# Kernel tuning notes

Hardware: AMD Instinct MI355X
Metric: run time of the kernel (lower is better)

The kernel has to match this reference:

```python
import jax, jax.numpy as jnp
import numpy as np

B, T, E, H = 1024, 200, 128, 128
N_ITEMS, N_CATS = 100000, 1000
LN_EPS = 1e-5


def _prelu(x, a):
    return jnp.where(x >= 0, x, a * x)


def _layernorm(x, g, b):
    m = x.mean(-1, keepdims=True)
    v = ((x - m) ** 2).mean(-1, keepdims=True)
    return (x - m) / jnp.sqrt(v + LN_EPS) * g + b


def setup_inputs() -> dict:
    key = jax.random.key(0)
    it = iter(jax.random.split(key, 64))
    nx = lambda: next(it)
    def lin(out_d, in_d):
        s = 1.0 / np.sqrt(in_d)
        return jax.random.uniform(nx(), (out_d, in_d), jnp.float32, -s, s)
    inp = {}
    inp['behavior_ids'] = jax.random.randint(nx(), (B, T), 0, N_ITEMS)
    inp['candidate_id'] = jax.random.randint(nx(), (B,), 0, N_ITEMS)
    inp['candidate_cat'] = jax.random.randint(nx(), (B,), 0, N_CATS)
    inp['dense_features'] = jax.random.normal(nx(), (B, 5), jnp.float32)
    inp['item_emb'] = (jax.random.normal(nx(), (N_ITEMS, E), jnp.float32) * 0.01).at[0].set(0.0)
    inp['cat_emb'] = (jax.random.normal(nx(), (N_CATS, E // 2), jnp.float32) * 0.01).at[0].set(0.0)
    # nn.GRU params (gate order r,z,n)
    inp['gru_wih'] = lin(3 * H, E)
    inp['gru_whh'] = lin(3 * H, H)
    inp['gru_bih'] = jnp.zeros((3 * H,), jnp.float32)
    inp['gru_bhh'] = jnp.zeros((3 * H,), jnp.float32)
    # auxiliary_net: Linear(H,E) -> ReLU -> Linear(E,1)
    inp['aux_w1'] = lin(E, H); inp['aux_b1'] = jnp.zeros((E,), jnp.float32)
    inp['aux_w2'] = lin(1, E); inp['aux_b2'] = jnp.zeros((1,), jnp.float32)
    # attention_mlp: Linear(3H,64) -> PReLU -> Linear(64,1)
    inp['att_w1'] = lin(64, 3 * H); inp['att_b1'] = jnp.zeros((64,), jnp.float32)
    inp['att_a'] = jnp.array(0.25, jnp.float32)
    inp['att_w2'] = lin(1, 64); inp['att_b2'] = jnp.zeros((1,), jnp.float32)
    # AUGRU gates: Linear(2H, H) each
    inp['wz'] = lin(H, 2 * H); inp['bz'] = jnp.zeros((H,), jnp.float32)
    inp['wr'] = lin(H, 2 * H); inp['br'] = jnp.zeros((H,), jnp.float32)
    inp['wh'] = lin(H, 2 * H); inp['bh'] = jnp.zeros((H,), jnp.float32)
    # dense_proj Linear(5,32)
    inp['dp_w'] = lin(32, 5); inp['dp_b'] = jnp.zeros((32,), jnp.float32)
    # MLP: 352 -> 256 -> 128 -> 64, each Linear + LayerNorm + PReLU
    dims = [H + E + E // 2 + 32, 256, 128, 64]
    for i in range(3):
        inp[f'm_w{i+1}'] = lin(dims[i + 1], dims[i])
        inp[f'm_b{i+1}'] = jnp.zeros((dims[i + 1],), jnp.float32)
        inp[f'ln_g{i+1}'] = jnp.ones((dims[i + 1],), jnp.float32)
        inp[f'ln_b{i+1}'] = jnp.zeros((dims[i + 1],), jnp.float32)
        inp[f'pa{i+1}'] = jnp.array(0.25, jnp.float32)
    # 3 task heads Linear(64,1), stacked
    inp['heads_w'] = lin(3, 64); inp['heads_b'] = jnp.zeros((3,), jnp.float32)
    return inp


def _forward_core(behavior_ids, candidate_id, candidate_cat, dense_features,
                  item_emb, cat_emb, gru_wih, gru_whh, gru_bih, gru_bhh,
                  aux_w1, aux_b1, aux_w2, aux_b2,
                  att_w1, att_b1, att_a, att_w2, att_b2,
                  wz, bz, wr, br, wh, bh, dp_w, dp_b,
                  m_w1, m_b1, ln_g1, ln_b1, pa1,
                  m_w2, m_b2, ln_g2, ln_b2, pa2,
                  m_w3, m_b3, ln_g3, ln_b3, pa3,
                  heads_w, heads_b):
    beh = item_emb[behavior_ids]            # [B,T,E]
    cand = item_emb[candidate_id]           # [B,E]
    catv = cat_emb[candidate_cat]           # [B,E//2]
    Bsz = beh.shape[0]
    Hd = gru_whh.shape[1]
    h0 = jnp.zeros((Bsz, Hd), beh.dtype)
    # --- interest extractor GRU (cuDNN GRU math, gate order r,z,n) ---
    xp = jnp.einsum('bte,ge->btg', beh, gru_wih) + gru_bih  # [B,T,3H]
    def gru_step(h, x):
        hp = h @ gru_whh.T + gru_bhh
        xr, xz, xn = jnp.split(x, 3, -1)
        hr, hz, hn = jnp.split(hp, 3, -1)
        r = jax.nn.sigmoid(xr + hr)
        z = jax.nn.sigmoid(xz + hz)
        n = jnp.tanh(xn + r * hn)
        hnew = (1 - z) * n + z * h
        return hnew, hnew
    _, hs = jax.lax.scan(gru_step, h0, jnp.swapaxes(xp, 0, 1))
    hs = jnp.swapaxes(hs, 0, 1)             # [B,T,H]
    # --- auxiliary logits ---
    aux = jax.nn.relu(hs[:, :-1] @ aux_w1.T + aux_b1) @ aux_w2.T + aux_b2  # [B,T-1,1]
    # --- attention (embed_dim == hidden_size so cand_proj == candidate_emb) ---
    ce = cand[:, None, :]
    att_in = jnp.concatenate([hs, jnp.broadcast_to(ce, hs.shape), hs * ce], -1)  # [B,T,3H]
    scores = (_prelu(att_in @ att_w1.T + att_b1, att_a) @ att_w2.T + att_b2)[..., 0]
    att = jax.nn.softmax(scores, axis=-1)   # [B,T]
    # --- AUGRU: attention-modulated update gate ---
    def augru_step(h, xs):
        x, a = xs                           # x: [B,H], a: [B]
        comb = jnp.concatenate([x, h], -1)
        z = jax.nn.sigmoid(comb @ wz.T + bz)
        r = jax.nn.sigmoid(comb @ wr.T + br)
        comb_r = jnp.concatenate([x, r * h], -1)
        ht = jnp.tanh(comb_r @ wh.T + bh)
        zp = a[:, None] * z
        return (1 - zp) * h + zp * ht, None
    hT, _ = jax.lax.scan(augru_step, h0, (jnp.swapaxes(hs, 0, 1), att.T))
    # --- fusion MLP (dropout is identity in eval) ---
    dense_out = dense_features @ dp_w.T + dp_b
    x = jnp.concatenate([hT, cand, catv, dense_out], -1)  # [B,352]
    for (w, b, g, be, a) in ((m_w1, m_b1, ln_g1, ln_b1, pa1),
                             (m_w2, m_b2, ln_g2, ln_b2, pa2),
                             (m_w3, m_b3, ln_g3, ln_b3, pa3)):
        x = _prelu(_layernorm(x @ w.T + b, g, be), a)
    preds = jax.nn.sigmoid(x @ heads_w.T + heads_b)  # [B,3] == 3 heads of [B,1]
    return preds, aux


def reference(behavior_ids, candidate_id, candidate_cat, dense_features,
              item_emb, cat_emb, gru_wih, gru_whh, gru_bih, gru_bhh,
              aux_w1, aux_b1, aux_w2, aux_b2,
              att_w1, att_b1, att_a, att_w2, att_b2,
              wz, bz, wr, br, wh, bh, dp_w, dp_b,
              m_w1, m_b1, ln_g1, ln_b1, pa1,
              m_w2, m_b2, ln_g2, ln_b2, pa2,
              m_w3, m_b3, ln_g3, ln_b3, pa3,
              heads_w, heads_b):
    return _forward_core(behavior_ids, candidate_id, candidate_cat, dense_features,
                         item_emb, cat_emb, gru_wih, gru_whh, gru_bih, gru_bhh,
                         aux_w1, aux_b1, aux_w2, aux_b2,
                         att_w1, att_b1, att_a, att_w2, att_b2,
                         wz, bz, wr, br, wh, bh, dp_w, dp_b,
                         m_w1, m_b1, ln_g1, ln_b1, pa1,
                         m_w2, m_b2, ln_g2, ln_b2, pa2,
                         m_w3, m_b3, ln_g3, ln_b3, pa3,
                         heads_w, heads_b)
```

## Files before the change

### kernel.cpp

```cpp
#include <hip/hip_runtime.h>


typedef __bf16 bf16;
typedef float f32x4 __attribute__((ext_vector_type(4)));
typedef __bf16 bf16x8 __attribute__((ext_vector_type(8)));
typedef __bf16 bf16x4 __attribute__((ext_vector_type(4)));

#define MFMA16(a, b, c) __builtin_amdgcn_mfma_f32_16x16x32_bf16((a), (b), (c), 0, 0, 0)

#define BATCH 1024
#define SEQT 200
#define F32_ONE 0x3F800000u

__device__ __forceinline__ float sigm(float x) {
  return __builtin_amdgcn_rcpf(1.0f + __expf(-x));
}
__device__ __forceinline__ float tanh_fast(float x) {
  float ax = fabsf(x);
  float t = 1.0f - 2.0f * __builtin_amdgcn_rcpf(__expf(2.0f * ax) + 1.0f);
  return copysignf(t, x);
}

__device__ __forceinline__ void bar_lgkm() {
  asm volatile("s_waitcnt lgkmcnt(0)\n\ts_barrier" ::: "memory");
}

__device__ __forceinline__ void dma16(const void* g, void* l) {
  __builtin_amdgcn_global_load_lds((__attribute__((address_space(1))) void*)g,
                                   (__attribute__((address_space(3))) void*)l,
                                   16, 0, 0);
}

template <typename DT> __device__ __forceinline__ float ldf(const DT* p, long i);
template <> __device__ __forceinline__ float ldf<bf16>(const bf16* p, long i) { return (float)p[i]; }
template <> __device__ __forceinline__ float ldf<float>(const float* p, long i) { return p[i]; }

template <typename DT> __device__ __forceinline__ bf16x8 ld8(const DT* p, long i);
template <> __device__ __forceinline__ bf16x8 ld8<bf16>(const bf16* p, long i) {
  return *(const bf16x8*)(p + i);
}
template <> __device__ __forceinline__ bf16x8 ld8<float>(const float* p, long i) {
  f32x4 a = *(const f32x4*)(p + i);
  f32x4 b = *(const f32x4*)(p + i + 4);
  bf16x8 r;
  r[0] = (bf16)a[0]; r[1] = (bf16)a[1]; r[2] = (bf16)a[2]; r[3] = (bf16)a[3];
  r[4] = (bf16)b[0]; r[5] = (bf16)b[1]; r[6] = (bf16)b[2]; r[7] = (bf16)b[3];
  return r;
}

template <typename DT>
__device__ __forceinline__ void prep_body(
    const int* __restrict__ cid, const int* __restrict__ ccat,
    const DT* __restrict__ dense, const DT* __restrict__ item_emb,
    const DT* __restrict__ cat_emb, const DT* __restrict__ dp_w,
    const DT* __restrict__ dp_b, bf16* __restrict__ candbuf, bf16* __restrict__ xf) {
  const int b = blockIdx.x;
  const int t = threadIdx.x;
  bf16 v = (bf16)ldf(item_emb, (long)cid[b] * 128 + t);
  candbuf[b * 128 + t] = v;
  xf[(long)b * 352 + 128 + t] = v;
  if (t < 64) xf[(long)b * 352 + 256 + t] = (bf16)ldf(cat_emb, (long)ccat[b] * 64 + t);
  if (t < 32) {
    float s = ldf(dp_b, t);
    for (int k = 0; k < 5; k++) s += ldf(dense, b * 5 + k) * ldf(dp_w, t * 5 + k);
    xf[(long)b * 352 + 320 + t] = (bf16)s;
  }
}
__global__ __launch_bounds__(128) void k_prep(
    const unsigned* __restrict__ disc, const int* cid, const int* ccat,
    const void* dense, const void* item_emb, const void* cat_emb,
    const void* dp_w, const void* dp_b, bf16* candbuf, bf16* xf) {
  if (*disc == F32_ONE)
    prep_body<float>(cid, ccat, (const float*)dense, (const float*)item_emb,
                     (const float*)cat_emb, (const float*)dp_w, (const float*)dp_b, candbuf, xf);
  else
    prep_body<bf16>(cid, ccat, (const bf16*)dense, (const bf16*)item_emb,
                    (const bf16*)cat_emb, (const bf16*)dp_w, (const bf16*)dp_b, candbuf, xf);
}

template <typename DT>
__device__ __forceinline__ void gru3_body(
    const int* __restrict__ ids, const DT* __restrict__ item_emb,
    const DT* __restrict__ wih, const DT* __restrict__ whh,
    const DT* __restrict__ bih, const DT* __restrict__ bhh, bf16* __restrict__ hs,
    bf16 (*hA)[16][136], bf16 (*xb)[4][16][136], char* raw) {
  const int b0 = blockIdx.x * 16;
  const int tid = threadIdx.x;
  const int w = tid >> 6, lane = tid & 63, l15 = lane & 15, quad = lane >> 4;
  const int nc = w * 16 + l15;

  for (int i = tid; i < 2 * 16 * 136; i += 512) ((bf16*)hA)[i] = (bf16)0.0f;

  bf16x8 wir[4], wiz[4], win_[4], whr[4], whz[4], whn[4];
#pragma unroll
  for (int k = 0; k < 4; k++) {
    const long off = k * 32 + quad * 8;
    wir[k] = ld8(wih, (long)nc * 128 + off);
    wiz[k] = ld8(wih, (long)(128 + nc) * 128 + off);
    win_[k] = ld8(wih, (long)(256 + nc) * 128 + off);
    whr[k] = ld8(whh, (long)nc * 128 + off);
    whz[k] = ld8(whh, (long)(128 + nc) * 128 + off);
    whn[k] = ld8(whh, (long)(256 + nc) * 128 + off);
  }
  const float br_s = ldf(bih, nc) + ldf(bhh, nc);
  const float bz_s = ldf(bih, 128 + nc) + ldf(bhh, 128 + nc);
  const float bxn_s = ldf(bih, 256 + nc);
  const float bhn_s = ldf(bhh, 256 + nc);

  const int idrow = (sizeof(DT) == 4) ? (tid >> 5) : ((tid >> 4) & 15);
  const int* idbase = ids + (long)(b0 + idrow) * SEQT;

  auto DMA = [&](const int4 id4) {
    if constexpr (sizeof(DT) == 4) {
#pragma unroll
      for (int j = 0; j < 4; j++)
        dma16((const char*)(item_emb + (long)((&id4.x)[j]) * 128) + (tid & 31) * 16,
              raw + (j * 512 + tid) * 16);
    } else {
#pragma unroll
      for (int j = 0; j < 2; j++) {
        const int slot = j * 2 + (tid >> 8);
        dma16((const char*)(item_emb + (long)((&id4.x)[slot]) * 128) + (tid & 15) * 16,
              raw + (j * 512 + tid) * 16);
      }
    }
  };
  auto CONV = [&](int buf) {
    if constexpr (sizeof(DT) == 4) {
      const float* rf = (const float*)raw;
#pragma unroll
      for (int h = 0; h < 4; h++) {
        const int e = h * 2048 + tid * 4;
        f32x4 a = *(const f32x4*)(rf + e);
        const int slot = e >> 11, row = (e >> 7) & 15, col = e & 127;
        bf16x4 o;
        o[0] = (bf16)a[0]; o[1] = (bf16)a[1]; o[2] = (bf16)a[2]; o[3] = (bf16)a[3];
        *(bf16x4*)&xb[buf][slot][row][col] = o;
      }
    } else {
      const bf16* rh = (const bf16*)raw;
#pragma unroll
      for (int h = 0; h < 2; h++) {
        const int e = h * 4096 + tid * 8;
        const int slot = e >> 11, row = (e >> 7) & 15, col = e & 127;
        *(bf16x8*)&xb[buf][slot][row][col] = *(const bf16x8*)(rh + e);
      }
    }
  };

  const int srow = tid >> 5, sch = (tid & 31) * 4;
  bf16* hsb = hs + ((long)(b0 + srow) * SEQT) * 128 + sch;

  float hreg[4] = {0.f, 0.f, 0.f, 0.f};
  const f32x4 z4 = {0.f, 0.f, 0.f, 0.f};

  int4 idv = *(const int4*)(idbase);
  DMA(idv);
  idv = *(const int4*)(idbase + 4);
  asm volatile("s_waitcnt vmcnt(1)" ::: "memory");
  __builtin_amdgcn_sched_barrier(0);
  __builtin_amdgcn_s_barrier();
  CONV(0);
  asm volatile("s_waitcnt lgkmcnt(0)" ::: "memory");
  __builtin_amdgcn_sched_barrier(0);
  __builtin_amdgcn_s_barrier();
  DMA(idv);
  idv = *(const int4*)(idbase + 8);

#define GRU_STEP(P, S)                                                         \
  {                                                                            \
    const int tt = t0 + (S);                                                   \
    bf16x8 af[4], xaf[4];                                                      \
    _Pragma("unroll") for (int k = 0; k < 4; k++) {                            \
      af[k] = *(const bf16x8*)&hA[P][l15][k * 32 + quad * 8];                  \
      xaf[k] = *(const bf16x8*)&xb[buf][S][l15][k * 32 + quad * 8];            \
    }                                                                          \
    { const int slot = tt ? tt - 1 : 0;                                        \
      bf16x4 hv = *(const bf16x4*)&hA[P][srow][sch];                           \
      *(bf16x4*)(hsb + (long)slot * 128) = hv; }                               \
    f32x4 ar = z4, az = z4, axn = z4, ahn = z4;                                \
    _Pragma("unroll") for (int k = 0; k < 4; k++) {                            \
      ar = MFMA16(xaf[k], wir[k], ar);                                         \
      az = MFMA16(xaf[k], wiz[k], az);                                         \
      axn = MFMA16(xaf[k], win_[k], axn);                                      \
    }                                                                          \
    _Pragma("unroll") for (int k = 0; k < 4; k++) {                            \
      ar = MFMA16(af[k], whr[k], ar);                                          \
      az = MFMA16(af[k], whz[k], az);                                          \
      ahn = MFMA16(af[k], whn[k], ahn);                                        \
    }                                                                          \
    _Pragma("unroll") for (int r = 0; r < 4; r++) {                            \
      float r_ = sigm(ar[r] + br_s);                                           \
      float z_ = sigm(az[r] + bz_s);                                           \
      float n_ = tanh_fast(axn[r] + bxn_s + r_ * (ahn[r] + bhn_s));            \
      float hnew = (1.0f - z_) * n_ + z_ * hreg[r];                            \
      hreg[r] = hnew;                                                          \
      hA[(P) ^ 1][quad * 4 + r][nc] = (bf16)hnew;                              \
    }                                                                          \
    bar_lgkm();                                                                \
  }

  for (int c = 0; c < 50; c++) {
    const int t0 = c * 4;
    const int buf = c & 1;
    GRU_STEP(0, 0) GRU_STEP(1, 1) GRU_STEP(0, 2) GRU_STEP(1, 3)
    if (c < 49) {
      asm volatile("s_waitcnt vmcnt(4)" ::: "memory");
      __builtin_amdgcn_sched_barrier(0);
      __builtin_amdgcn_s_barrier();
      CONV((c + 1) & 1);
      asm volatile("s_waitcnt lgkmcnt(0)" ::: "memory");
      __builtin_amdgcn_sched_barrier(0);
      __builtin_amdgcn_s_barrier();
      if (c < 48) {
        DMA(idv);
        int nid = (c + 3) * 4; if (nid > 196) nid = 196;
        idv = *(const int4*)(idbase + nid);
      }
    }
  }
#undef GRU_STEP
  { bf16x4 hv = *(const bf16x4*)&hA[0][srow][sch];
    *(bf16x4*)(hsb + (long)(SEQT - 1) * 128) = hv; }
}
__global__ __launch_bounds__(512, 1) void k_gru3(
    const unsigned* __restrict__ disc, const int* ids, const void* item_emb,
    const void* wih, const void* whh, const void* bih, const void* bhh, bf16* hs) {
  __shared__ __align__(16) bf16 hA[2][16][136];
  __shared__ __align__(16) bf16 xb[2][4][16][136];
  __shared__ __align__(16) char raw[32768];
  if (*disc == F32_ONE)
    gru3_body<float>(ids, (const float*)item_emb, (const float*)wih, (const float*)whh,
                     (const float*)bih, (const float*)bhh, hs, hA, xb, raw);
  else
    gru3_body<bf16>(ids, (const bf16*)item_emb, (const bf16*)wih, (const bf16*)whh,
                    (const bf16*)bih, (const bf16*)bhh, hs, hA, xb, raw);
}

template <typename DT>
__device__ __forceinline__ void attaux_body(
    const bf16* __restrict__ hs, const int* __restrict__ cid,
    const DT* __restrict__ item_emb,
    const DT* __restrict__ aw1, const DT* __restrict__ ab1,
    const DT* __restrict__ aw2, const DT* __restrict__ ab2,
    const DT* __restrict__ tw1, const DT* __restrict__ tb1, const DT* __restrict__ ta,
    const DT* __restrict__ tw2, const DT* __restrict__ tb2,
    float* __restrict__ sc, float* __restrict__ outaux,
    bf16 (*As)[64][128], float (*scPt)[64], float (*scPa)[64]) {
  const int t0 = blockIdx.x * 64;
  const int b0 = blockIdx.y * 16;
  const int tid = threadIdx.x, w = tid >> 6, lane = tid & 63, l15 = lane & 15, quad = lane >> 4;

  const int tn = w * 16 + l15;
  bf16x8 wth[4], wtc[4], wthc[4], wa0[4], wa1[4];
#pragma unroll
  for (int k = 0; k < 4; k++) {
    const long off = k * 32 + quad * 8;
    wth[k]  = ld8(tw1, (long)tn * 384 + off);
    wtc[k]  = ld8(tw1, (long)tn * 384 + 128 + off);
    wthc[k] = ld8(tw1, (long)tn * 384 + 256 + off);
    wa0[k]  = ld8(aw1, (long)((2 * w) * 16 + l15) * 128 + off);
    wa1[k]  = ld8(aw1, (long)((2 * w + 1) * 16 + l15) * 128 + off);
  }
  const float tb1c = ldf(tb1, tn), tw2c = ldf(tw2, tn);
  const float ab1c0 = ldf(ab1, (2 * w) * 16 + l15), aw2c0 = ldf(aw2, (2 * w) * 16 + l15);
  const float ab1c1 = ldf(ab1, (2 * w + 1) * 16 + l15), aw2c1 = ldf(aw2, (2 * w + 1) * 16 + l15);
  const float aP = ldf(ta, 0), tb2s = ldf(tb2, 0), ab2s = ldf(ab2, 0);

  auto DMA = [&](int b, int buf) {
#pragma unroll
    for (int c = 0; c < 4; c++) {
      const int idx = c * 256 + tid;
      const int row = idx >> 4, p = idx & 15;
      int t = t0 + row; if (t > SEQT - 1) t = SEQT - 1;
      const bf16* src = hs + ((long)b * SEQT + t) * 128 + ((p ^ (row & 7)) * 8);
      dma16(src, (char*)(&As[buf][0][0]) + idx * 16);
    }
  };
  auto CANDLD = [&](int b, bf16x8* cf) {
#pragma unroll
    for (int k = 0; k < 4; k++)
      cf[k] = ld8(item_emb, (long)cid[b] * 128 + k * 32 + quad * 8);
  };

  const f32x4 z4 = {0.f, 0.f, 0.f, 0.f};
  bf16x8 candA[4], candB[4];
  DMA(b0, 0);
  CANDLD(b0, candA);
  asm volatile("s_waitcnt vmcnt(0)" ::: "memory");
  __builtin_amdgcn_sched_barrier(0);
  __builtin_amdgcn_s_barrier();

#define AA_STEP(BI, CUSE, CPF)                                                 \
  {                                                                            \
    const int b = b0 + (BI);                                                   \
    const int buf = (BI) & 1;                                                  \
    if ((BI) + 1 < 16) { DMA(b + 1, buf ^ 1); CANDLD(b + 1, CPF); }            \
    _Pragma("unroll") for (int m = 0; m < 4; m++) {                            \
      const bf16* arow = &As[buf][m * 16 + l15][0];                            \
      bf16x8 af[4], hcf[4];                                                    \
      _Pragma("unroll") for (int k = 0; k < 4; k++)                            \
        af[k] = *(const bf16x8*)((const char*)arow +                           \
                                 (((k * 4 + quad) ^ (l15 & 7)) << 4));         \
      _Pragma("unroll") for (int k = 0; k < 4; k++)                            \
      _Pragma("unroll") for (int j = 0; j < 8; j++)                            \
        hcf[k][j] = (bf16)((float)af[k][j] * (float)CUSE[k][j]);               \
      f32x4 at = z4, aa0 = z4, aa1 = z4;                                       \
      _Pragma("unroll") for (int k = 0; k < 4; k++) {                          \
        at = MFMA16(af[k], wth[k], at);                                        \
        at = MFMA16(CUSE[k], wtc[k], at);                                      \
        at = MFMA16(hcf[k], wthc[k], at);                                      \
        aa0 = MFMA16(af[k], wa0[k], aa0);                                      \
        aa1 = MFMA16(af[k], wa1[k], aa1);                                      \
      }                                                                        \
      float tp[4], ap[4];                                                      \
      _Pragma("unroll") for (int r = 0; r < 4; r++) {                          \
        float y = at[r] + tb1c;                                                \
        y = (y >= 0.f) ? y : aP * y;                                           \
        tp[r] = y * tw2c;                                                      \
        float y0 = aa0[r] + ab1c0;                                             \
        float y1 = aa1[r] + ab1c1;                                             \
        ap[r] = (y0 > 0.f ? y0 : 0.f) * aw2c0 + (y1 > 0.f ? y1 : 0.f) * aw2c1; \
      }                                                                        \
      _Pragma("unroll") for (int mm = 1; mm < 16; mm <<= 1)                    \
      _Pragma("unroll") for (int r = 0; r < 4; r++) {                          \
        tp[r] += __shfl_xor(tp[r], mm, 64);                                    \
        ap[r] += __shfl_xor(ap[r], mm, 64);                                    \
      }                                                                        \
      if (l15 == 0) {                                                          \
        *(float4*)&scPt[w][m * 16 + quad * 4] =                                \
            make_float4(tp[0], tp[1], tp[2], tp[3]);                           \
        *(float4*)&scPa[w][m * 16 + quad * 4] =                                \
            make_float4(ap[0], ap[1], ap[2], ap[3]);                           \
      }                                                                        \
    }                                                                          \
    bar_lgkm();                                                                \
    if (tid < 64) {                                                            \
      int t = t0 + tid;                                                        \
      if (t < SEQT) {                                                          \
        float s = scPt[0][tid] + scPt[1][tid] + scPt[2][tid] + scPt[3][tid];   \
        sc[(long)b * SEQT + t] = s + tb2s;                                     \
      }                                                                        \
    } else if (tid < 128) {                                                    \
      int tt2 = tid - 64, t = t0 + tt2;                                        \
      if (t < SEQT - 1) {                                                      \
        float s = scPa[0][tt2] + scPa[1][tt2] + scPa[2][tt2] + scPa[3][tt2];   \
        outaux[(long)b * 199 + t] = s + ab2s;                                  \
      }                                                                        \
    }                                                                          \
    asm volatile("s_waitcnt vmcnt(0) lgkmcnt(0)" ::: "memory");                \
    __builtin_amdgcn_sched_barrier(0);                                         \
    __builtin_amdgcn_s_barrier();                                              \
  }

  for (int bi = 0; bi < 16; bi += 2) {
    AA_STEP(bi, candA, candB)
    AA_STEP(bi + 1, candB, candA)
  }
#undef AA_STEP
}
__global__ __launch_bounds__(256, 1) void k_attaux(
    const unsigned* __restrict__ disc, const bf16* hs, const int* cid,
    const void* item_emb,
    const void* aw1, const void* ab1, const void* aw2, const void* ab2,
    const void* tw1, const void* tb1, const void* ta, const void* tw2, const void* tb2,
    float* sc, float* outaux) {
  __shared__ __align__(16) bf16 As[2][64][128];
  __shared__ __align__(16) float scPt[4][64];
  __shared__ __align__(16) float scPa[4][64];
  if (*disc == F32_ONE)
    attaux_body<float>(hs, cid, (const float*)item_emb,
                       (const float*)aw1, (const float*)ab1, (const float*)aw2, (const float*)ab2,
                       (const float*)tw1, (const float*)tb1, (const float*)ta,
                       (const float*)tw2, (const float*)tb2, sc, outaux, As, scPt, scPa);
  else
    attaux_body<bf16>(hs, cid, (const bf16*)item_emb,
                      (const bf16*)aw1, (const bf16*)ab1, (const bf16*)aw2, (const bf16*)ab2,
                      (const bf16*)tw1, (const bf16*)tb1, (const bf16*)ta,
                      (const bf16*)tw2, (const bf16*)tb2, sc, outaux, As, scPt, scPa);
}

__global__ __launch_bounds__(256) void k_softmax(float* __restrict__ sc) {
  const int b = blockIdx.x, tid = threadIdx.x;
  __shared__ float red[256];
  float v = (tid < SEQT) ? sc[(long)b * SEQT + tid] : -1e30f;
  red[tid] = v; __syncthreads();
  for (int s = 128; s > 0; s >>= 1) { if (tid < s) red[tid] = fmaxf(red[tid], red[tid + s]); __syncthreads(); }
  float mx = red[0]; __syncthreads();
  float e = (tid < SEQT) ? __expf(v - mx) : 0.f;
  red[tid] = e; __syncthreads();
  for (int s = 128; s > 0; s >>= 1) { if (tid < s) red[tid] += red[tid + s]; __syncthreads(); }
  float inv = 1.0f / red[0];
  if (tid < SEQT) sc[(long)b * SEQT + tid] = e * inv;
}

template <typename DT>
__device__ __forceinline__ void augru3_body(
    const bf16* __restrict__ hsrc, const float* __restrict__ att,
    const DT* __restrict__ wz, const DT* __restrict__ wr, const DT* __restrict__ wh,
    const DT* __restrict__ bzv, const DT* __restrict__ brv, const DT* __restrict__ bhv,
    bf16* __restrict__ xf_out,
    bf16 (*hA)[16][136], bf16 (*rhA)[136], float (*attL)[201],
    bf16 (*xb)[4][16][136], char* raw) {
  const int b0 = blockIdx.x * 16;
  const int tid = threadIdx.x;
  const int w = tid >> 6, lane = tid & 63, l15 = lane & 15, quad = lane >> 4;
  const int nc = w * 16 + l15;

  for (int i = tid; i < 2 * 16 * 136; i += 512) ((bf16*)hA)[i] = (bf16)0.0f;
  for (int i = tid; i < 16 * SEQT; i += 512) {
    int r = i / SEQT, c = i - r * SEQT;
    attL[r][c] = att[(long)(b0 + r) * SEQT + c];
  }

  bf16x8 wzx[4], wzh[4], wrx[4], wrh[4], whx[4], whh_[4];
#pragma unroll
  for (int k = 0; k < 4; k++) {
    const long off = k * 32 + quad * 8;
    wzx[k] = ld8(wz, (long)nc * 256 + off);
    wzh[k] = ld8(wz, (long)nc * 256 + 128 + off);
    wrx[k] = ld8(wr, (long)nc * 256 + off);
    wrh[k] = ld8(wr, (long)nc * 256 + 128 + off);
    whx[k] = ld8(wh, (long)nc * 256 + off);
    whh_[k] = ld8(wh, (long)nc * 256 + 128 + off);
  }
  const float bz_s = ldf(bzv, nc);
  const float br_s = ldf(brv, nc);
  const float bh_s = ldf(bhv, nc);

  auto DMA = [&](int t0) {
#pragma unroll
    for (int j = 0; j < 2; j++) {
      const int slot = j * 2 + (tid >> 8);
      const int row = (tid >> 4) & 15;
      const bf16* src = hsrc + ((long)(b0 + row) * SEQT + t0 + slot) * 128 + (tid & 15) * 8;
      dma16(src, raw + (j * 512 + tid) * 16);
    }
  };
  auto CONV = [&](int buf) {
    const bf16* rh = (const bf16*)raw;
#pragma unroll
    for (int h = 0; h < 2; h++) {
      const int e = h * 4096 + tid * 8;
      const int slot = e >> 11, row = (e >> 7) & 15, col = e & 127;
      *(bf16x8*)&xb[buf][slot][row][col] = *(const bf16x8*)(rh + e);
    }
  };

  float hreg[4] = {0.f, 0.f, 0.f, 0.f};
  const f32x4 z4 = {0.f, 0.f, 0.f, 0.f};

  DMA(0);
  asm volatile("s_waitcnt vmcnt(0)" ::: "memory");
  __builtin_amdgcn_sched_barrier(0);
  __builtin_amdgcn_s_barrier();
  CONV(0);
  asm volatile("s_waitcnt lgkmcnt(0)" ::: "memory");
  __builtin_amdgcn_sched_barrier(0);
  __builtin_amdgcn_s_barrier();
  DMA(4);

#define AUGRU_STEP(P, S)                                                       \
  {                                                                            \
    const int tt = t0 + (S);                                                   \
    bf16x8 af[4], xaf[4];                                                      \
    _Pragma("unroll") for (int k = 0; k < 4; k++) {                            \
      af[k] = *(const bf16x8*)&hA[P][l15][k * 32 + quad * 8];                  \
      xaf[k] = *(const bf16x8*)&xb[buf][S][l15][k * 32 + quad * 8];            \
    }                                                                          \
    f32x4 az = z4, ar = z4, axh = z4;                                          \
    _Pragma("unroll") for (int k = 0; k < 4; k++) {                            \
      az = MFMA16(xaf[k], wzx[k], az);                                         \
      ar = MFMA16(xaf[k], wrx[k], ar);                                         \
      axh = MFMA16(xaf[k], whx[k], axh);                                       \
    }                                                                          \
    _Pragma("unroll") for (int k = 0; k < 4; k++) {                            \
      az = MFMA16(af[k], wzh[k], az);                                          \
      ar = MFMA16(af[k], wrh[k], ar);                                          \
    }                                                                          \
    float zp[4];                                                               \
    _Pragma("unroll") for (int r = 0; r < 4; r++) {                            \
      float a_ = attL[quad * 4 + r][tt];                                       \
      float z_ = sigm(az[r] + bz_s);                                           \
      float r_ = sigm(ar[r] + br_s);                                           \
      zp[r] = a_ * z_;                                                         \
      rhA[quad * 4 + r][nc] = (bf16)(r_ * hreg[r]);                            \
    }                                                                          \
    bar_lgkm();                                                                \
    bf16x8 rf[4];                                                              \
    _Pragma("unroll") for (int k = 0; k < 4; k++)                              \
      rf[k] = *(const bf16x8*)&rhA[l15][k * 32 + quad * 8];                    \
    f32x4 ahh = axh;                                                           \
    _Pragma("unroll") for (int k = 0; k < 4; k++)                              \
      ahh = MFMA16(rf[k], whh_[k], ahh);                                       \
    _Pragma("unroll") for (int r = 0; r < 4; r++) {                            \
      float ht = tanh_fast(ahh[r] + bh_s);                                     \
      float hnew = (1.f - zp[r]) * hreg[r] + zp[r] * ht;                       \
      hreg[r] = hnew;                                                          \
      hA[(P) ^ 1][quad * 4 + r][nc] = (bf16)hnew;                              \
    }                                                                          \
    bar_lgkm();                                                                \
  }

  for (int c = 0; c < 50; c++) {
    const int t0 = c * 4;
    const int buf = c & 1;
    AUGRU_STEP(0, 0) AUGRU_STEP(1, 1) AUGRU_STEP(0, 2) AUGRU_STEP(1, 3)
    if (c < 49) {
      asm volatile("s_waitcnt vmcnt(0)" ::: "memory");
      __builtin_amdgcn_sched_barrier(0);
      __builtin_amdgcn_s_barrier();
      CONV((c + 1) & 1);
      asm volatile("s_waitcnt lgkmcnt(0)" ::: "memory");
      __builtin_amdgcn_sched_barrier(0);
      __builtin_amdgcn_s_barrier();
      if (c < 48) DMA((c + 2) * 4);
    }
  }
#undef AUGRU_STEP
#pragma unroll
  for (int r = 0; r < 4; r++)
    xf_out[(long)(b0 + quad * 4 + r) * 352 + nc] = (bf16)hreg[r];
}
__global__ __launch_bounds__(512, 1) void k_augru3(
    const unsigned* __restrict__ disc, const bf16* hsrc, const float* att,
    const void* wz, const void* wr, const void* wh,
    const void* bzv, const void* brv, const void* bhv, bf16* xf_out) {
  __shared__ __align__(16) bf16 hA[2][16][136];
  __shared__ __align__(16) bf16 rhA[16][136];
  __shared__ __align__(16) float attL[16][201];
  __shared__ __align__(16) bf16 xb[2][4][16][136];
  __shared__ __align__(16) char raw[16384];
  if (*disc == F32_ONE)
    augru3_body<float>(hsrc, att, (const float*)wz, (const float*)wr, (const float*)wh,
                       (const float*)bzv, (const float*)brv, (const float*)bhv, xf_out,
                       hA, rhA, attL, xb, raw);
  else
    augru3_body<bf16>(hsrc, att, (const bf16*)wz, (const bf16*)wr, (const bf16*)wh,
                      (const bf16*)bzv, (const bf16*)brv, (const bf16*)bhv, xf_out,
                      hA, rhA, attL, xb, raw);
}

template <typename DT>
__device__ __forceinline__ void mlp_body(
    const bf16* __restrict__ xf,
    const DT* __restrict__ w1, const DT* __restrict__ b1, const DT* __restrict__ g1, const DT* __restrict__ be1, const DT* __restrict__ pa1,
    const DT* __restrict__ w2, const DT* __restrict__ b2, const DT* __restrict__ g2, const DT* __restrict__ be2, const DT* __restrict__ pa2,
    const DT* __restrict__ w3, const DT* __restrict__ b3, const DT* __restrict__ g3, const DT* __restrict__ be3, const DT* __restrict__ pa3,
    const DT* __restrict__ hw, const DT* __restrict__ hb, float* __restrict__ preds,
    float (*xs)[352], float (*ys)[256]) {
  const int tid = threadIdx.x, w = tid >> 6, lane = tid & 63;
  const int b = blockIdx.x * 4 + w;
  for (int i = lane; i < 352; i += 64) xs[w][i] = (float)xf[(long)b * 352 + i];
  __syncthreads();
  float acc1[4];
#pragma unroll
  for (int oi = 0; oi < 4; oi++) {
    int o = lane + 64 * oi;
    float s = ldf(b1, o);
    for (int k = 0; k < 352; k += 8) {
      bf16x8 wv = ld8(w1, (long)o * 352 + k);
#pragma unroll
      for (int j = 0; j < 8; j++) s += xs[w][k + j] * (float)wv[j];
    }
    acc1[oi] = s;
  }
  float sm = acc1[0] + acc1[1] + acc1[2] + acc1[3];
#pragma unroll
  for (int m = 1; m < 64; m <<= 1) sm += __shfl_xor(sm, m, 64);
  float mean = sm * (1.0f / 256.0f);
  float vs = 0.f;
#pragma unroll
  for (int oi = 0; oi < 4; oi++) { float d = acc1[oi] - mean; vs += d * d; }
#pragma unroll
  for (int m = 1; m < 64; m <<= 1) vs += __shfl_xor(vs, m, 64);
  float rstd = rsqrtf(vs * (1.0f / 256.0f) + 1e-5f);
  float a1 = ldf(pa1, 0);
#pragma unroll
  for (int oi = 0; oi < 4; oi++) {
    int o = lane + 64 * oi;
    float y = (acc1[oi] - mean) * rstd * ldf(g1, o) + ldf(be1, o);
    ys[w][o] = (y >= 0.f) ? y : a1 * y;
  }
  __syncthreads();
  float acc2[2];
#pragma unroll
  for (int oi = 0; oi < 2; oi++) {
    int o = lane + 64 * oi;
    float s = ldf(b2, o);
    for (int k = 0; k < 256; k += 8) {
      bf16x8 wv = ld8(w2, (long)o * 256 + k);
#pragma unroll
      for (int j = 0; j < 8; j++) s += ys[w][k + j] * (float)wv[j];
    }
    acc2[oi] = s;
  }
  sm = acc2[0] + acc2[1];
#pragma unroll
  for (int m = 1; m < 64; m <<= 1) sm += __shfl_xor(sm, m, 64);
  mean = sm * (1.0f / 128.0f);
  vs = 0.f;
#pragma unroll
  for (int oi = 0; oi < 2; oi++) { float d = acc2[oi] - mean; vs += d * d; }
#pragma unroll
  for (int m = 1; m < 64; m <<= 1) vs += __shfl_xor(vs, m, 64);
  rstd = rsqrtf(vs * (1.0f / 128.0f) + 1e-5f);
  float a2 = ldf(pa2, 0);
  __syncthreads();
#pragma unroll
  for (int oi = 0; oi < 2; oi++) {
    int o = lane + 64 * oi;
    float y = (acc2[oi] - mean) * rstd * ldf(g2, o) + ldf(be2, o);
    xs[w][o] = (y >= 0.f) ? y : a2 * y;
  }
  __syncthreads();
  float s3 = ldf(b3, lane);
  for (int k = 0; k < 128; k += 8) {
    bf16x8 wv = ld8(w3, (long)lane * 128 + k);
#pragma unroll
    for (int j = 0; j < 8; j++) s3 += xs[w][k + j] * (float)wv[j];
  }
  sm = s3;
#pragma unroll
  for (int m = 1; m < 64; m <<= 1) sm += __shfl_xor(sm, m, 64);
  mean = sm * (1.0f / 64.0f);
  float d3 = s3 - mean;
  vs = d3 * d3;
#pragma unroll
  for (int m = 1; m < 64; m <<= 1) vs += __shfl_xor(vs, m, 64);
  rstd = rsqrtf(vs * (1.0f / 64.0f) + 1e-5f);
  float a3 = ldf(pa3, 0);
  float y3 = d3 * rstd * ldf(g3, lane) + ldf(be3, lane);
  y3 = (y3 >= 0.f) ? y3 : a3 * y3;
  ys[w][lane] = y3;
  __syncthreads();
  if (lane < 3) {
    float s = ldf(hb, lane);
    for (int k = 0; k < 64; k++) s += ys[w][k] * ldf(hw, lane * 64 + k);
    preds[(long)b * 3 + lane] = sigm(s);
  }
}
__global__ __launch_bounds__(256) void k_mlp(
    const unsigned* __restrict__ disc, const bf16* xf,
    const void* w1, const void* b1, const void* g1, const void* be1, const void* pa1,
    const void* w2, const void* b2, const void* g2, const void* be2, const void* pa2,
    const void* w3, const void* b3, const void* g3, const void* be3, const void* pa3,
    const void* hw, const void* hb, float* preds) {
  __shared__ float xs[4][352];
  __shared__ float ys[4][256];
  if (*disc == F32_ONE)
    mlp_body<float>(xf,
        (const float*)w1, (const float*)b1, (const float*)g1, (const float*)be1, (const float*)pa1,
        (const float*)w2, (const float*)b2, (const float*)g2, (const float*)be2, (const float*)pa2,
        (const float*)w3, (const float*)b3, (const float*)g3, (const float*)be3, (const float*)pa3,
        (const float*)hw, (const float*)hb, preds, xs, ys);
  else
    mlp_body<bf16>(xf,
        (const bf16*)w1, (const bf16*)b1, (const bf16*)g1, (const bf16*)be1, (const bf16*)pa1,
        (const bf16*)w2, (const bf16*)b2, (const bf16*)g2, (const bf16*)be2, (const bf16*)pa2,
        (const bf16*)w3, (const bf16*)b3, (const bf16*)g3, (const bf16*)be3, (const bf16*)pa3,
        (const bf16*)hw, (const bf16*)hb, preds, xs, ys);
}

extern "C" void kernel_launch(void* const* d_in, const int* in_sizes, int n_in,
                              void* d_out, int out_size, void* d_ws, size_t ws_size,
                              hipStream_t stream) {
  const int* behavior_ids = (const int*)d_in[0];
  const int* candidate_id = (const int*)d_in[1];
  const int* candidate_cat = (const int*)d_in[2];
  const void* dense = d_in[3];
  const void* item_emb = d_in[4];
  const void* cat_emb = d_in[5];
  const void* gru_wih = d_in[6];
  const void* gru_whh = d_in[7];
  const void* gru_bih = d_in[8];
  const void* gru_bhh = d_in[9];
  const void* aux_w1 = d_in[10];
  const void* aux_b1 = d_in[11];
  const void* aux_w2 = d_in[12];
  const void* aux_b2 = d_in[13];
  const void* att_w1 = d_in[14];
  const void* att_b1 = d_in[15];
  const void* att_a = d_in[16];
  const void* att_w2 = d_in[17];
  const void* att_b2 = d_in[18];
  const void* wz = d_in[19];
  const void* bz = d_in[20];
  const void* wr = d_in[21];
  const void* br = d_in[22];
  const void* wh = d_in[23];
  const void* bh = d_in[24];
  const void* dp_w = d_in[25];
  const void* dp_b = d_in[26];
  const void* m_w1 = d_in[27];
  const void* m_b1 = d_in[28];
  const void* ln_g1 = d_in[29];
  const void* ln_b1 = d_in[30];
  const void* pa1 = d_in[31];
  const void* m_w2 = d_in[32];
  const void* m_b2 = d_in[33];
  const void* ln_g2 = d_in[34];
  const void* ln_b2 = d_in[35];
  const void* pa2 = d_in[36];
  const void* m_w3 = d_in[37];
  const void* m_b3 = d_in[38];
  const void* ln_g3 = d_in[39];
  const void* ln_b3 = d_in[40];
  const void* pa3 = d_in[41];
  const void* heads_w = d_in[42];
  const void* heads_b = d_in[43];
  (void)in_sizes; (void)n_in; (void)out_size; (void)ws_size;

  const unsigned* disc = (const unsigned*)ln_g1;

  char* ws = (char*)d_ws;
  bf16* HS = (bf16*)(ws);
  float* SC = (float*)(ws + 52428800L);
  bf16* CAND = (bf16*)(ws + 53248000L);
  bf16* XF = (bf16*)(ws + 53510144L);
  float* OUT = (float*)d_out;

  k_prep<<<BATCH, 128, 0, stream>>>(disc, candidate_id, candidate_cat, dense, item_emb,
                                    cat_emb, dp_w, dp_b, CAND, XF);
  k_gru3<<<64, 512, 0, stream>>>(disc, behavior_ids, item_emb, gru_wih, gru_whh,
                                 gru_bih, gru_bhh, HS);
  k_attaux<<<dim3(4, 64), 256, 0, stream>>>(disc, HS, candidate_id, item_emb,
                                            aux_w1, aux_b1, aux_w2, aux_b2,
                                            att_w1, att_b1, att_a, att_w2, att_b2,
                                            SC, OUT + 3072);
  k_softmax<<<BATCH, 256, 0, stream>>>(SC);
  k_augru3<<<64, 512, 0, stream>>>(disc, HS, SC, wz, wr, wh, bz, br, bh, XF);
  k_mlp<<<256, 256, 0, stream>>>(disc, XF,
      m_w1, m_b1, ln_g1, ln_b1, pa1,
      m_w2, m_b2, ln_g2, ln_b2, pa2,
      m_w3, m_b3, ln_g3, ln_b3, pa3,
      heads_w, heads_b, OUT);
}
```

Before: 727.2 us.

## Pre-cast embedding table to bf16 and DMA swizzled rows directly into LDS

```diff
diff --git a/kernel.cpp b/kernel.cpp
--- a/kernel.cpp
+++ b/kernel.cpp
@@ -46,6 +46,17 @@
   r[0] = (bf16)a[0]; r[1] = (bf16)a[1]; r[2] = (bf16)a[2]; r[3] = (bf16)a[3];
   r[4] = (bf16)b[0]; r[5] = (bf16)b[1]; r[6] = (bf16)b[2]; r[7] = (bf16)b[3];
   return r;
+}
+
+template <typename DT>
+__device__ __forceinline__ void cast_body(const DT* __restrict__ src, bf16* __restrict__ dst) {
+  const long i = ((long)blockIdx.x * 256 + threadIdx.x) * 8;
+  if (i < 100000L * 128) *(bf16x8*)(dst + i) = ld8(src, i);
+}
+__global__ __launch_bounds__(256) void k_cast(
+    const unsigned* __restrict__ disc, const void* src, bf16* dst) {
+  if (*disc == F32_ONE) cast_body<float>((const float*)src, dst);
+  else                  cast_body<bf16>((const bf16*)src, dst);
 }
 
 template <typename DT>
@@ -79,11 +90,11 @@
 }
 
 template <typename DT>
-__device__ __forceinline__ void gru3_body(
-    const int* __restrict__ ids, const DT* __restrict__ item_emb,
+__device__ __forceinline__ void gru5_body(
+    const int* __restrict__ ids, const bf16* __restrict__ ieb,
     const DT* __restrict__ wih, const DT* __restrict__ whh,
     const DT* __restrict__ bih, const DT* __restrict__ bhh, bf16* __restrict__ hs,
-    bf16 (*hA)[16][136], bf16 (*xb)[4][16][136], char* raw) {
+    bf16 (*hA)[16][136], bf16 (*xb)[4][16][128]) {
   const int b0 = blockIdx.x * 16;
   const int tid = threadIdx.x;
   const int w = tid >> 6, lane = tid & 63, l15 = lane & 15, quad = lane >> 4;
@@ -107,46 +118,18 @@
   const float bxn_s = ldf(bih, 256 + nc);
   const float bhn_s = ldf(bhh, 256 + nc);
 
-  const int idrow = (sizeof(DT) == 4) ? (tid >> 5) : ((tid >> 4) & 15);
+  const int idrow = (tid >> 4) & 15;
   const int* idbase = ids + (long)(b0 + idrow) * SEQT;
-
-  auto DMA = [&](const int4 id4) {
-    if constexpr (sizeof(DT) == 4) {
-#pragma unroll
-      for (int j = 0; j < 4; j++)
-        dma16((const char*)(item_emb + (long)((&id4.x)[j]) * 128) + (tid & 31) * 16,
-              raw + (j * 512 + tid) * 16);
-    } else {
-#pragma unroll
-      for (int j = 0; j < 2; j++) {
-        const int slot = j * 2 + (tid >> 8);
-        dma16((const char*)(item_emb + (long)((&id4.x)[slot]) * 128) + (tid & 15) * 16,
-              raw + (j * 512 + tid) * 16);
-      }
+  const int srcoff = ((tid & 15) ^ (idrow & 7)) * 8;
+
+  auto DMA = [&](const int4 id4, int buf) {
+#pragma unroll
+    for (int j = 0; j < 2; j++) {
+      const int slot = j * 2 + (tid >> 8);
+      dma16(ieb + (long)((&id4.x)[slot]) * 128 + srcoff,
+            (char*)&xb[buf][0][0][0] + (j * 512 + tid) * 16);
     }
   };
-  auto CONV = [&](int buf) {
-    if constexpr (sizeof(DT) == 4) {
-      const float* rf = (const float*)raw;
-#pragma unroll
-      for (int h = 0; h < 4; h++) {
-        const int e = h * 2048 + tid * 4;
-        f32x4 a = *(const f32x4*)(rf + e);
-        const int slot = e >> 11, row = (e >> 7) & 15, col = e & 127;
-        bf16x4 o;
-        o[0] = (bf16)a[0]; o[1] = (bf16)a[1]; o[2] = (bf16)a[2]; o[3] = (bf16)a[3];
-        *(bf16x4*)&xb[buf][slot][row][col] = o;
-      }
-    } else {
-      const bf16* rh = (const bf16*)raw;
-#pragma unroll
-      for (int h = 0; h < 2; h++) {
-        const int e = h * 4096 + tid * 8;
-        const int slot = e >> 11, row = (e >> 7) & 15, col = e & 127;
-        *(bf16x8*)&xb[buf][slot][row][col] = *(const bf16x8*)(rh + e);
-      }
-    }
-  };
 
   const int srow = tid >> 5, sch = (tid & 31) * 4;
   bf16* hsb = hs + ((long)(b0 + srow) * SEQT) * 128 + sch;
@@ -155,25 +138,20 @@
   const f32x4 z4 = {0.f, 0.f, 0.f, 0.f};
 
   int4 idv = *(const int4*)(idbase);
-  DMA(idv);
+  DMA(idv, 0);
   idv = *(const int4*)(idbase + 4);
   asm volatile("s_waitcnt vmcnt(1)" ::: "memory");
   __builtin_amdgcn_sched_barrier(0);
   __builtin_amdgcn_s_barrier();
-  CONV(0);
-  asm volatile("s_waitcnt lgkmcnt(0)" ::: "memory");
-  __builtin_amdgcn_sched_barrier(0);
-  __builtin_amdgcn_s_barrier();
-  DMA(idv);
-  idv = *(const int4*)(idbase + 8);
-
-#define GRU_STEP(P, S)                                                         \
+
+#define GRU_STEP(P, S, WAITC)                                                  \
   {                                                                            \
     const int tt = t0 + (S);                                                   \
     bf16x8 af[4], xaf[4];                                                      \
     _Pragma("unroll") for (int k = 0; k < 4; k++) {                            \
       af[k] = *(const bf16x8*)&hA[P][l15][k * 32 + quad * 8];                  \
-      xaf[k] = *(const bf16x8*)&xb[buf][S][l15][k * 32 + quad * 8];            \
+      xaf[k] = *(const bf16x8*)((const char*)&xb[buf][S][0][0] + l15 * 256 +   \
+                                ((((k << 2) + quad) ^ (l15 & 7)) << 4));       \
     }                                                                          \
     { const int slot = tt ? tt - 1 : 0;                                        \
       bf16x4 hv = *(const bf16x4*)&hA[P][srow][sch];                           \
@@ -197,44 +175,39 @@
       hreg[r] = hnew;                                                          \
       hA[(P) ^ 1][quad * 4 + r][nc] = (bf16)hnew;                              \
     }                                                                          \
-    bar_lgkm();                                                                \
+    if (WAITC) {                                                               \
+       \
+      asm volatile("s_waitcnt vmcnt(5) lgkmcnt(0)\n\ts_barrier" ::: "memory"); \
+    } else {                                                                   \
+      bar_lgkm();                                                              \
+    }                                                                          \
   }
 
   for (int c = 0; c < 50; c++) {
     const int t0 = c * 4;
     const int buf = c & 1;
-    GRU_STEP(0, 0) GRU_STEP(1, 1) GRU_STEP(0, 2) GRU_STEP(1, 3)
     if (c < 49) {
-      asm volatile("s_waitcnt vmcnt(4)" ::: "memory");
-      __builtin_amdgcn_sched_barrier(0);
-      __builtin_amdgcn_s_barrier();
-      CONV((c + 1) & 1);
-      asm volatile("s_waitcnt lgkmcnt(0)" ::: "memory");
-      __builtin_amdgcn_sched_barrier(0);
-      __builtin_amdgcn_s_barrier();
-      if (c < 48) {
-        DMA(idv);
-        int nid = (c + 3) * 4; if (nid > 196) nid = 196;
-        idv = *(const int4*)(idbase + nid);
-      }
+      DMA(idv, buf ^ 1);
+      int nid = (c + 2) * 4; if (nid > 196) nid = 196;
+      idv = *(const int4*)(idbase + nid);
     }
+    GRU_STEP(0, 0, 0) GRU_STEP(1, 1, 0) GRU_STEP(0, 2, 0) GRU_STEP(1, 3, (c < 49))
   }
 #undef GRU_STEP
   { bf16x4 hv = *(const bf16x4*)&hA[0][srow][sch];
     *(bf16x4*)(hsb + (long)(SEQT - 1) * 128) = hv; }
 }
-__global__ __launch_bounds__(512, 1) void k_gru3(
-    const unsigned* __restrict__ disc, const int* ids, const void* item_emb,
+__global__ __launch_bounds__(512, 1) void k_gru5(
+    const unsigned* __restrict__ disc, const int* ids, const bf16* ieb,
     const void* wih, const void* whh, const void* bih, const void* bhh, bf16* hs) {
   __shared__ __align__(16) bf16 hA[2][16][136];
-  __shared__ __align__(16) bf16 xb[2][4][16][136];
-  __shared__ __align__(16) char raw[32768];
+  __shared__ __align__(16) bf16 xb[2][4][16][128];
   if (*disc == F32_ONE)
-    gru3_body<float>(ids, (const float*)item_emb, (const float*)wih, (const float*)whh,
-                     (const float*)bih, (const float*)bhh, hs, hA, xb, raw);
+    gru5_body<float>(ids, ieb, (const float*)wih, (const float*)whh,
+                     (const float*)bih, (const float*)bhh, hs, hA, xb);
   else
-    gru3_body<bf16>(ids, (const bf16*)item_emb, (const bf16*)wih, (const bf16*)whh,
-                    (const bf16*)bih, (const bf16*)bhh, hs, hA, xb, raw);
+    gru5_body<bf16>(ids, ieb, (const bf16*)wih, (const bf16*)whh,
+                    (const bf16*)bih, (const bf16*)bhh, hs, hA, xb);
 }
 
 template <typename DT>
@@ -395,13 +368,13 @@
 }
 
 template <typename DT>
-__device__ __forceinline__ void augru3_body(
+__device__ __forceinline__ void augru5_body(
     const bf16* __restrict__ hsrc, const float* __restrict__ att,
     const DT* __restrict__ wz, const DT* __restrict__ wr, const DT* __restrict__ wh,
     const DT* __restrict__ bzv, const DT* __restrict__ brv, const DT* __restrict__ bhv,
     bf16* __restrict__ xf_out,
     bf16 (*hA)[16][136], bf16 (*rhA)[136], float (*attL)[201],
-    bf16 (*xb)[4][16][136], char* raw) {
+    bf16 (*xb)[4][16][128]) {
   const int b0 = blockIdx.x * 16;
   const int tid = threadIdx.x;
   const int w = tid >> 6, lane = tid & 63, l15 = lane & 15, quad = lane >> 4;
@@ -428,45 +401,33 @@
   const float br_s = ldf(brv, nc);
   const float bh_s = ldf(bhv, nc);
 
-  auto DMA = [&](int t0) {
+  const int drow = (tid >> 4) & 15;
+  const int srcoff = ((tid & 15) ^ (drow & 7)) * 8;
+  auto DMA = [&](int t0, int buf) {
 #pragma unroll
     for (int j = 0; j < 2; j++) {
       const int slot = j * 2 + (tid >> 8);
-      const int row = (tid >> 4) & 15;
-      const bf16* src = hsrc + ((long)(b0 + row) * SEQT + t0 + slot) * 128 + (tid & 15) * 8;
-      dma16(src, raw + (j * 512 + tid) * 16);
+      dma16(hsrc + ((long)(b0 + drow) * SEQT + t0 + slot) * 128 + srcoff,
+            (char*)&xb[buf][0][0][0] + (j * 512 + tid) * 16);
     }
   };
-  auto CONV = [&](int buf) {
-    const bf16* rh = (const bf16*)raw;
-#pragma unroll
-    for (int h = 0; h < 2; h++) {
-      const int e = h * 4096 + tid * 8;
-      const int slot = e >> 11, row = (e >> 7) & 15, col = e & 127;
-      *(bf16x8*)&xb[buf][slot][row][col] = *(const bf16x8*)(rh + e);
-    }
-  };
 
   float hreg[4] = {0.f, 0.f, 0.f, 0.f};
   const f32x4 z4 = {0.f, 0.f, 0.f, 0.f};
 
-  DMA(0);
+  DMA(0, 0);
   asm volatile("s_waitcnt vmcnt(0)" ::: "memory");
   __builtin_amdgcn_sched_barrier(0);
   __builtin_amdgcn_s_barrier();
-  CONV(0);
-  asm volatile("s_waitcnt lgkmcnt(0)" ::: "memory");
-  __builtin_amdgcn_sched_barrier(0);
-  __builtin_amdgcn_s_barrier();
-  DMA(4);
-
-#define AUGRU_STEP(P, S)                                                       \
+
+#define AUGRU_STEP(P, S, WAITC)                                                \
   {                                                                            \
     const int tt = t0 + (S);                                                   \
     bf16x8 af[4], xaf[4];                                                      \
     _Pragma("unroll") for (int k = 0; k < 4; k++) {                            \
       af[k] = *(const bf16x8*)&hA[P][l15][k * 32 + quad * 8];                  \
-      xaf[k] = *(const bf16x8*)&xb[buf][S][l15][k * 32 + quad * 8];            \
+      xaf[k] = *(const bf16x8*)((const char*)&xb[buf][S][0][0] + l15 * 256 +   \
+                                ((((k << 2) + quad) ^ (l15 & 7)) << 4));       \
     }                                                                          \
     f32x4 az = z4, ar = z4, axh = z4;                                          \
     _Pragma("unroll") for (int k = 0; k < 4; k++) {                            \
@@ -499,46 +460,41 @@
       hreg[r] = hnew;                                                          \
       hA[(P) ^ 1][quad * 4 + r][nc] = (bf16)hnew;                              \
     }                                                                          \
-    bar_lgkm();                                                                \
+    if (WAITC) {                                                               \
+                     \
+      asm volatile("s_waitcnt vmcnt(0) lgkmcnt(0)\n\ts_barrier" ::: "memory"); \
+    } else {                                                                   \
+      bar_lgkm();                                                              \
+    }                                                                          \
   }
 
   for (int c = 0; c < 50; c++) {
     const int t0 = c * 4;
     const int buf = c & 1;
-    AUGRU_STEP(0, 0) AUGRU_STEP(1, 1) AUGRU_STEP(0, 2) AUGRU_STEP(1, 3)
-    if (c < 49) {
-      asm volatile("s_waitcnt vmcnt(0)" ::: "memory");
-      __builtin_amdgcn_sched_barrier(0);
-      __builtin_amdgcn_s_barrier();
-      CONV((c + 1) & 1);
-      asm volatile("s_waitcnt lgkmcnt(0)" ::: "memory");
-      __builtin_amdgcn_sched_barrier(0);
-      __builtin_amdgcn_s_barrier();
-      if (c < 48) DMA((c + 2) * 4);
-    }
+    if (c < 49) DMA((c + 1) * 4, buf ^ 1);
+    AUGRU_STEP(0, 0, 0) AUGRU_STEP(1, 1, 0) AUGRU_STEP(0, 2, 0) AUGRU_STEP(1, 3, (c < 49))
   }
 #undef AUGRU_STEP
 #pragma unroll
   for (int r = 0; r < 4; r++)
     xf_out[(long)(b0 + quad * 4 + r) * 352 + nc] = (bf16)hreg[r];
 }
-__global__ __launch_bounds__(512, 1) void k_augru3(
+__global__ __launch_bounds__(512, 1) void k_augru5(
     const unsigned* __restrict__ disc, const bf16* hsrc, const float* att,
     const void* wz, const void* wr, const void* wh,
     const void* bzv, const void* brv, const void* bhv, bf16* xf_out) {
   __shared__ __align__(16) bf16 hA[2][16][136];
   __shared__ __align__(16) bf16 rhA[16][136];
   __shared__ __align__(16) float attL[16][201];
-  __shared__ __align__(16) bf16 xb[2][4][16][136];
-  __shared__ __align__(16) char raw[16384];
+  __shared__ __align__(16) bf16 xb[2][4][16][128];
   if (*disc == F32_ONE)
-    augru3_body<float>(hsrc, att, (const float*)wz, (const float*)wr, (const float*)wh,
+    augru5_body<float>(hsrc, att, (const float*)wz, (const float*)wr, (const float*)wh,
                        (const float*)bzv, (const float*)brv, (const float*)bhv, xf_out,
-                       hA, rhA, attL, xb, raw);
+                       hA, rhA, attL, xb);
   else
-    augru3_body<bf16>(hsrc, att, (const bf16*)wz, (const bf16*)wr, (const bf16*)wh,
+    augru5_body<bf16>(hsrc, att, (const bf16*)wz, (const bf16*)wr, (const bf16*)wh,
                       (const bf16*)bzv, (const bf16*)brv, (const bf16*)bhv, xf_out,
-                      hA, rhA, attL, xb, raw);
+                      hA, rhA, attL, xb);
 }
 
 template <typename DT>
@@ -718,18 +674,20 @@
   float* SC = (float*)(ws + 52428800L);
   bf16* CAND = (bf16*)(ws + 53248000L);
   bf16* XF = (bf16*)(ws + 53510144L);
+  bf16* IEB = (bf16*)(ws + 54231040L);
   float* OUT = (float*)d_out;
 
+  k_cast<<<6250, 256, 0, stream>>>(disc, item_emb, IEB);
   k_prep<<<BATCH, 128, 0, stream>>>(disc, candidate_id, candidate_cat, dense, item_emb,
                                     cat_emb, dp_w, dp_b, CAND, XF);
-  k_gru3<<<64, 512, 0, stream>>>(disc, behavior_ids, item_emb, gru_wih, gru_whh,
+  k_gru5<<<64, 512, 0, stream>>>(disc, behavior_ids, IEB, gru_wih, gru_whh,
                                  gru_bih, gru_bhh, HS);
   k_attaux<<<dim3(4, 64), 256, 0, stream>>>(disc, HS, candidate_id, item_emb,
                                             aux_w1, aux_b1, aux_w2, aux_b2,
                                             att_w1, att_b1, att_a, att_w2, att_b2,
                                             SC, OUT + 3072);
   k_softmax<<<BATCH, 256, 0, stream>>>(SC);
-  k_augru3<<<64, 512, 0, stream>>>(disc, HS, SC, wz, wr, wh, bz, br, bh, XF);
+  k_augru5<<<64, 512, 0, stream>>>(disc, HS, SC, wz, wr, wh, bz, br, bh, XF);
   k_mlp<<<256, 256, 0, stream>>>(disc, XF,
       m_w1, m_b1, ln_g1, ln_b1, pa1,
       m_w2, m_b2, ln_g2, ln_b2, pa2,
```

Result: no change. 733.9 us (+0.9%).
